# Optimization experiments

Hardware: AMD Instinct MI355X
Metric: run time of the kernel (lower is better)

The kernel has to match this reference:

```python
import jax, jax.numpy as jnp
import numpy as np

C = 256
CQK = C // 8  # 32


def setup_inputs() -> dict:
    key = jax.random.key(0)
    ks = jax.random.split(key, 7)
    x = jax.random.normal(ks[0], (8, C, 64, 64), dtype=jnp.float32)
    s = 1.0 / np.sqrt(C)
    Wq = jax.random.normal(ks[1], (CQK, C), dtype=jnp.float32) * s
    bq = jnp.zeros((CQK,), dtype=jnp.float32)
    Wk = jax.random.normal(ks[2], (CQK, C), dtype=jnp.float32) * s
    bk = jnp.zeros((CQK,), dtype=jnp.float32)
    Wv = jax.random.normal(ks[3], (C, C), dtype=jnp.float32) * s
    bv = jnp.zeros((C,), dtype=jnp.float32)
    gamma = jnp.zeros((1,), dtype=jnp.float32)
    return {"x": x, "Wq": Wq, "bq": bq, "Wk": Wk, "bk": bk, "Wv": Wv, "bv": bv, "gamma": gamma}


def reference(x, Wq, bq, Wk, bk, Wv, bv, gamma):
    B, Cc, H, W = x.shape
    N = H * W
    xf = x.reshape(B, Cc, N)  # [B, C, N]
    # 1x1 convs == channel matmuls
    q = jnp.einsum('oc,bcn->bon', Wq, xf) + bq[None, :, None]  # [B, C//8, N]
    k = jnp.einsum('oc,bcn->bon', Wk, xf) + bk[None, :, None]  # [B, C//8, N]
    v = jnp.einsum('oc,bcn->bon', Wv, xf) + bv[None, :, None]  # [B, C, N]
    scale = float(Cc // 8) ** (-0.5)
    # attention[b, i, j] over keys j (softmax on last dim)
    scores = jnp.einsum('bon,bom->bnm', q, k) * scale  # [B, N, N]
    attn = jax.nn.softmax(scores, axis=-1)
    # out[b,c,i] = sum_j v[b,c,j] * attn[b,i,j]
    out = jnp.einsum('bcj,bij->bci', v, attn).reshape(B, Cc, H, W)
    return gamma * out + x
```

## Files before the change

### kernel.cpp

```cpp
#include <hip/hip_runtime.h>
#include <hip/hip_bf16.h>
#include <math.h>

#define B_   8
#define C_   256
#define N_   4096
#define QSCALE_L2E 0.2550541451582815f
#define DEFER_THR  11.5f

typedef __attribute__((ext_vector_type(8))) short bf16x8;
typedef __attribute__((ext_vector_type(4))) float f32x4;

__device__ __forceinline__ unsigned short bfu(float f) {
    __hip_bfloat16 h = __float2bfloat16(f);
    return __builtin_bit_cast(unsigned short, h);
}
__device__ __forceinline__ unsigned cvtpk(float lo, float hi) {
    unsigned r;
    asm("v_cvt_pk_bf16_f32 %0, %1, %2" : "=v"(r) : "v"(lo), "v"(hi));
    return r;
}

__global__ __launch_bounds__(256) void w_prep(
    const float* __restrict__ Wq, const float* __restrict__ Wk,
    const float* __restrict__ Wv, unsigned short* __restrict__ wbf)
{
    const int i = blockIdx.x * 256 + threadIdx.x;
    const int off = i * 4;
    float4 f;
    if (off < 32 * C_)            f = *reinterpret_cast<const float4*>(Wq + off);
    else if (off < 64 * C_)       f = *reinterpret_cast<const float4*>(Wk + off - 32 * C_);
    else                          f = *reinterpret_cast<const float4*>(Wv + off - 64 * C_);
    ushort4 u;
    u.x = bfu(f.x); u.y = bfu(f.y); u.z = bfu(f.z); u.w = bfu(f.w);
    *reinterpret_cast<ushort4*>(wbf + off) = u;
}

__global__ __launch_bounds__(256, 2) void qkv_proj_mfma(
    const float* __restrict__ x, const unsigned short* __restrict__ wbf,
    const float* __restrict__ bq, const float* __restrict__ bk,
    const float* __restrict__ bv,
    unsigned short* __restrict__ q, unsigned short* __restrict__ k,
    unsigned short* __restrict__ v)
{
    const int b = blockIdx.y, n0 = blockIdx.x * 64;
    const int t = threadIdx.x;
    const int w = t >> 6, l = t & 63;
    const int li = l & 15, g = l >> 4;

    __shared__ unsigned short xT[64 * 256];
    __shared__ unsigned short qkS[2 * 64 * 32];

    {
        const int n = t & 63;
        const int cq0 = t >> 6;
        const float* xb = x + ((size_t)b * C_) * N_ + n0 + n;
        #pragma unroll 4
        for (int s = 0; s < 16; ++s) {
            const int cq = cq0 + 4 * s;
            const float f0 = xb[(size_t)(cq * 4 + 0) * N_];
            const float f1 = xb[(size_t)(cq * 4 + 1) * N_];
            const float f2 = xb[(size_t)(cq * 4 + 2) * N_];
            const float f3 = xb[(size_t)(cq * 4 + 3) * N_];
            ushort4 pk;
            pk.x = bfu(f0); pk.y = bfu(f1); pk.z = bfu(f2); pk.w = bfu(f3);
            const int byte = n * 512 + (((cq >> 1) ^ (n & 7)) << 4) + (cq & 1) * 8;
            *reinterpret_cast<ushort4*>(reinterpret_cast<char*>(xT) + byte) = pk;
        }
    }
    __syncthreads();

    const unsigned short* wq_bf = wbf;
    const unsigned short* wk_bf = wbf + 32 * C_;
    const unsigned short* wv_bf = wbf + 64 * C_;

    const unsigned short* wqk_bf = (w < 2) ? wq_bf : wk_bf;
    const float* bqk = (w < 2) ? bq : bk;
    const float qscl = (w < 2) ? QSCALE_L2E : 1.0f;
    const int mt0 = (w & 1) * 2;
    const int ov0 = w * 64;

    f32x4 accv[4][4];
    f32x4 accq[2][2];
    const f32x4 z4 = {0.f, 0.f, 0.f, 0.f};
    #pragma unroll
    for (int a = 0; a < 4; ++a)
        #pragma unroll
        for (int c2 = 0; c2 < 4; ++c2) accv[a][c2] = z4;
    #pragma unroll
    for (int a = 0; a < 2; ++a)
        #pragma unroll
        for (int c2 = 0; c2 < 2; ++c2) accq[a][c2] = z4;

    #pragma unroll 2
    for (int kk = 0; kk < 8; ++kk) {
        bf16x8 xf[4];
        #pragma unroll
        for (int nt = 0; nt < 4; ++nt) {
            const int row = nt * 16 + li;
            const int byte = row * 512 + (((kk * 4 + g) ^ (row & 7)) << 4);
            xf[nt] = *reinterpret_cast<const bf16x8*>(
                reinterpret_cast<const char*>(xT) + byte);
        }
        #pragma unroll
        for (int ot = 0; ot < 4; ++ot) {
            const bf16x8 wV = *reinterpret_cast<const bf16x8*>(
                wv_bf + (size_t)(ov0 + ot * 16 + li) * C_ + kk * 32 + g * 8);
            #pragma unroll
            for (int nt = 0; nt < 4; ++nt)
                accv[nt][ot] = __builtin_amdgcn_mfma_f32_16x16x32_bf16(
                    xf[nt], wV, accv[nt][ot], 0, 0, 0);
        }
        #pragma unroll
        for (int ot = 0; ot < 2; ++ot) {
            const bf16x8 wA = *reinterpret_cast<const bf16x8*>(
                wqk_bf + (size_t)(ot * 16 + li) * C_ + kk * 32 + g * 8);
            #pragma unroll
            for (int m2 = 0; m2 < 2; ++m2)
                accq[ot][m2] = __builtin_amdgcn_mfma_f32_16x16x32_bf16(
                    wA, xf[mt0 + m2], accq[ot][m2], 0, 0, 0);
        }
    }

    __syncthreads();

    {
        const int qk = (w < 2) ? 0 : 1;
        #pragma unroll
        for (int ot = 0; ot < 2; ++ot) {
            const int d0 = ot * 16 + 4 * g;
            const float4 b4 = *reinterpret_cast<const float4*>(bqk + d0);
            const int slot = ot * 4 + g;
            #pragma unroll
            for (int m2 = 0; m2 < 2; ++m2) {
                const int n = (mt0 + m2) * 16 + li;
                ushort4 s4;
                s4.x = bfu((accq[ot][m2][0] + b4.x) * qscl);
                s4.y = bfu((accq[ot][m2][1] + b4.y) * qscl);
                s4.z = bfu((accq[ot][m2][2] + b4.z) * qscl);
                s4.w = bfu((accq[ot][m2][3] + b4.w) * qscl);
                const int byte = qk * 4096 + n * 64 + ((slot ^ (n & 7)) << 3);
                *reinterpret_cast<ushort4*>(reinterpret_cast<char*>(qkS) + byte) = s4;
            }
        }
    }
    {
        #pragma unroll
        for (int ot = 0; ot < 4; ++ot) {
            const int o = ov0 + ot * 16 + li;
            const float bias = bv[o];
            #pragma unroll
            for (int nt = 0; nt < 4; ++nt) {
                ushort4 s4;
                s4.x = bfu(accv[nt][ot][0] + bias);
                s4.y = bfu(accv[nt][ot][1] + bias);
                s4.z = bfu(accv[nt][ot][2] + bias);
                s4.w = bfu(accv[nt][ot][3] + bias);
                const int slot = nt * 4 + g;
                const int byte = o * 128 + ((slot ^ (o & 7)) << 3);
                *reinterpret_cast<ushort4*>(reinterpret_cast<char*>(xT) + byte) = s4;
            }
        }
    }
    __syncthreads();

    {
        const char* qks = reinterpret_cast<const char*>(qkS);
        #pragma unroll
        for (int qk = 0; qk < 2; ++qk) {
            const int n = t >> 2, s2 = (t & 3) * 2;
            const int byteA = qk * 4096 + n * 64 + (((s2    ) ^ (n & 7)) << 3);
            const int byteB = qk * 4096 + n * 64 + (((s2 + 1) ^ (n & 7)) << 3);
            const uint2 lo = *reinterpret_cast<const uint2*>(qks + byteA);
            const uint2 hi = *reinterpret_cast<const uint2*>(qks + byteB);
            uint4 val = make_uint4(lo.x, lo.y, hi.x, hi.y);
            unsigned short* dst = (qk == 0) ? q : k;
            *reinterpret_cast<uint4*>(dst + ((size_t)b * N_ + n0) * 32 + t * 8) = val;
        }
    }
    {
        const char* vs = reinterpret_cast<const char*>(xT);
        #pragma unroll
        for (int p2 = 0; p2 < 8; ++p2) {
            const int o = p2 * 32 + (t >> 3);
            const int s2 = (t & 7) * 2;
            const int byteA = o * 128 + (((s2    ) ^ (o & 7)) << 3);
            const int byteB = o * 128 + (((s2 + 1) ^ (o & 7)) << 3);
            const uint2 lo = *reinterpret_cast<const uint2*>(vs + byteA);
            const uint2 hi = *reinterpret_cast<const uint2*>(vs + byteB);
            uint4 val = make_uint4(lo.x, lo.y, hi.x, hi.y);
            *reinterpret_cast<uint4*>(v + ((size_t)b * C_ + o) * N_ + n0 + (t & 7) * 8) = val;
        }
    }
}

__global__ __launch_bounds__(256, 2) void attn_mfma(
    const unsigned short* __restrict__ q, const unsigned short* __restrict__ k,
    const unsigned short* __restrict__ v,
    const float* __restrict__ x, const float* __restrict__ gamma,
    float* __restrict__ out)
{
    const int id = blockIdx.x;
    const int b = id & 7;
    const int i0 = (id >> 3) * 64;
    const int t = threadIdx.x;
    const int w = t >> 6, l = t & 63;
    const int li = l & 15, g = l >> 4;

    __shared__ unsigned short kT[2][64 * 32];
    __shared__ unsigned short vT[2][256 * 64];

    const unsigned short* qb = q + (size_t)b * N_ * 32;
    const unsigned short* kb = k + (size_t)b * N_ * 32;
    const unsigned short* vb = v + ((size_t)b * C_) * N_;

    const bf16x8 qf = *reinterpret_cast<const bf16x8*>(
        qb + (size_t)(i0 + w * 16 + li) * 32 + g * 8);

    f32x4 acc[16];
    const f32x4 z4 = {0.f, 0.f, 0.f, 0.f};
    #pragma unroll
    for (int a = 0; a < 16; ++a) acc[a] = z4;

    float m_run = -3.0e38f;
    float l_part = 0.f;

    const int jr = t >> 2, sl = t & 3;
    const int jt_s = jr >> 4, gg = (jr >> 2) & 3, rr = jr & 3;
    const int jperm = (jt_s >> 1) * 32 + (jt_s & 1) * 4 + gg * 8 + rr;
    const int s_src = sl ^ (jr & 3);
    const int koff_sh = jperm * 32 + s_src * 8;
    const unsigned voffK = (unsigned)(koff_sh * 2);
    const int kdst_byte = t * 16;

    const int vrow0 = w * 16 + (l >> 2);
    const int vchunk = l & 3;
    unsigned voffVb[4];
    int vdst[4][2];
    #pragma unroll
    for (int p = 0; p < 4; ++p) {
        const int row = vrow0 + p * 64;
        voffVb[p] = (unsigned)(((size_t)row * N_ + vchunk * 16) * 2);
        const int s0 = vchunk * 2;
        vdst[p][0] = row * 128 + (((s0    ) ^ (row & 7)) << 4);
        vdst[p][1] = row * 128 + (((s0 + 1) ^ (row & 7)) << 4);
    }

    union PB { unsigned wo[4]; bf16x8 v8; };

    {
        const bf16x8 k0 = *reinterpret_cast<const bf16x8*>(
            reinterpret_cast<const char*>(kb) + voffK);
        *reinterpret_cast<bf16x8*>(reinterpret_cast<char*>(&kT[0][0]) + kdst_byte) = k0;
        #pragma unroll
        for (int p = 0; p < 4; ++p) {
            const char* src = reinterpret_cast<const char*>(vb) + voffVb[p];
            const bf16x8 a0 = *reinterpret_cast<const bf16x8*>(src);
            const bf16x8 a1 = *reinterpret_cast<const bf16x8*>(src + 16);
            *reinterpret_cast<bf16x8*>(reinterpret_cast<char*>(&vT[0][0]) + vdst[p][0]) = a0;
            *reinterpret_cast<bf16x8*>(reinterpret_cast<char*>(&vT[0][0]) + vdst[p][1]) = a1;
        }
    }
    __syncthreads();

    for (int jj = 0; jj < 64; ++jj) {
        const int cur = jj & 1, nxt = cur ^ 1;
        const bool pf = (jj + 1 < 64);

        bf16x8 knx;
        bf16x8 vnx[4][2];
        if (pf) {
            const unsigned short* sbk = kb + (size_t)(jj + 1) * 64 * 32;
            asm volatile("global_load_dwordx4 %0, %1, %2"
                         : "=v"(knx) : "v"(voffK), "s"(sbk));
            const unsigned short* sbv = vb + (size_t)(jj + 1) * 64;
            #pragma unroll
            for (int p = 0; p < 4; ++p)
                asm volatile("global_load_dwordx4 %0, %2, %3\n\t"
                             "global_load_dwordx4 %1, %2, %3 offset:16"
                             : "=v"(vnx[p][0]), "=v"(vnx[p][1])
                             : "v"(voffVb[p]), "s"(sbv));
            __builtin_amdgcn_sched_barrier(0);
        }

        f32x4 sT[4];
        {
            const char* kbuf = reinterpret_cast<const char*>(&kT[cur][0]);
            #pragma unroll
            for (int jt = 0; jt < 4; ++jt) {
                const int row = jt * 16 + li;
                const bf16x8 kA = *reinterpret_cast<const bf16x8*>(
                    kbuf + row * 64 + ((g ^ (row & 3)) << 4));
                sT[jt] = __builtin_amdgcn_mfma_f32_16x16x32_bf16(kA, qf, z4, 0, 0, 0);
            }
        }

        float mx = fmaxf(fmaxf(fmaxf(sT[0][0], sT[0][1]), fmaxf(sT[0][2], sT[0][3])),
                         fmaxf(fmaxf(sT[1][0], sT[1][1]), fmaxf(sT[1][2], sT[1][3])));
        mx = fmaxf(mx, fmaxf(fmaxf(fmaxf(sT[2][0], sT[2][1]), fmaxf(sT[2][2], sT[2][3])),
                             fmaxf(fmaxf(sT[3][0], sT[3][1]), fmaxf(sT[3][2], sT[3][3]))));
        if (__any(mx > m_run + DEFER_THR)) {
            float mw = fmaxf(mx, __shfl_xor(mx, 16));
            mw = fmaxf(mw, __shfl_xor(mw, 32));
            const float mnew = fmaxf(m_run, mw);
            const float f = __builtin_amdgcn_exp2f(m_run - mnew);
            m_run = mnew;
            l_part *= f;
            #pragma unroll
            for (int ct = 0; ct < 16; ++ct) acc[ct] *= f;
        }
        #pragma unroll
        for (int jt = 0; jt < 4; ++jt)
            #pragma unroll
            for (int r = 0; r < 4; ++r)
                sT[jt][r] = __builtin_amdgcn_exp2f(sT[jt][r] - m_run);
        const f32x4 sv = (sT[0] + sT[1]) + (sT[2] + sT[3]);
        l_part += (sv[0] + sv[1]) + (sv[2] + sv[3]);

        PB pb0, pb1;
        pb0.wo[0] = cvtpk(sT[0][0], sT[0][1]); pb0.wo[1] = cvtpk(sT[0][2], sT[0][3]);
        pb0.wo[2] = cvtpk(sT[1][0], sT[1][1]); pb0.wo[3] = cvtpk(sT[1][2], sT[1][3]);
        pb1.wo[0] = cvtpk(sT[2][0], sT[2][1]); pb1.wo[1] = cvtpk(sT[2][2], sT[2][3]);
        pb1.wo[2] = cvtpk(sT[3][0], sT[3][1]); pb1.wo[3] = cvtpk(sT[3][2], sT[3][3]);

        __builtin_amdgcn_s_setprio(1);
        {
            const char* vbuf = reinterpret_cast<const char*>(&vT[cur][0]);
            #pragma unroll
            for (int ct = 0; ct < 16; ++ct) {
                const int vrow = ct * 16 + li;
                const bf16x8 vA0 = *reinterpret_cast<const bf16x8*>(
                    vbuf + vrow * 128 + (((g    ) ^ (vrow & 7)) << 4));
                const bf16x8 vA1 = *reinterpret_cast<const bf16x8*>(
                    vbuf + vrow * 128 + (((4 + g) ^ (vrow & 7)) << 4));
                acc[ct] = __builtin_amdgcn_mfma_f32_16x16x32_bf16(vA0, pb0.v8, acc[ct], 0, 0, 0);
                acc[ct] = __builtin_amdgcn_mfma_f32_16x16x32_bf16(vA1, pb1.v8, acc[ct], 0, 0, 0);
            }
        }
        __builtin_amdgcn_s_setprio(0);

        if (pf) {
            asm volatile("s_waitcnt vmcnt(0)" ::: "memory");
            __builtin_amdgcn_sched_barrier(0);
            *reinterpret_cast<bf16x8*>(
                reinterpret_cast<char*>(&kT[nxt][0]) + kdst_byte) = knx;
            char* vd = reinterpret_cast<char*>(&vT[nxt][0]);
            #pragma unroll
            for (int p = 0; p < 4; ++p) {
                *reinterpret_cast<bf16x8*>(vd + vdst[p][0]) = vnx[p][0];
                *reinterpret_cast<bf16x8*>(vd + vdst[p][1]) = vnx[p][1];
            }
        }
        __syncthreads();
    }

    float l_tot = l_part;
    l_tot += __shfl_xor(l_tot, 16);
    l_tot += __shfl_xor(l_tot, 32);
    const float linv = 1.0f / l_tot;

    const float gm = gamma[0];
    const int i = i0 + w * 16 + li;
    const float* xb2 = x + ((size_t)b * C_) * N_ + i;
    float* ob = out + ((size_t)b * C_) * N_ + i;
    #pragma unroll
    for (int ct = 0; ct < 16; ++ct) {
        #pragma unroll
        for (int r = 0; r < 4; ++r) {
            const int c = ct * 16 + 4 * g + r;
            const size_t off = (size_t)c * N_;
            ob[off] = gm * acc[ct][r] * linv + xb2[off];
        }
    }
}

extern "C" void kernel_launch(void* const* d_in, const int* in_sizes, int n_in,
                              void* d_out, int out_size, void* d_ws, size_t ws_size,
                              hipStream_t stream) {
    const float* x     = (const float*)d_in[0];
    const float* Wq    = (const float*)d_in[1];
    const float* bq    = (const float*)d_in[2];
    const float* Wk    = (const float*)d_in[3];
    const float* bk    = (const float*)d_in[4];
    const float* Wv    = (const float*)d_in[5];
    const float* bv    = (const float*)d_in[6];
    const float* gamma = (const float*)d_in[7];
    float* out = (float*)d_out;

    unsigned short* q   = (unsigned short*)d_ws;
    unsigned short* k   = q + (size_t)B_ * N_ * 32;
    unsigned short* v   = k + (size_t)B_ * N_ * 32;
    unsigned short* wbf = v + (size_t)B_ * C_ * N_;

    dim3 grid(N_ / 64, B_);
    w_prep<<<80, 256, 0, stream>>>(Wq, Wk, Wv, wbf);
    qkv_proj_mfma<<<grid, 256, 0, stream>>>(x, wbf, bq, bk, bv, q, k, v);
    attn_mfma<<<512, 256, 0, stream>>>(q, k, v, x, gamma, out);
}
```

Measured before the change: 156.2 us.

## Process two query tiles per wave to reuse K/V LDS fragments

Each wave now handles 32 query rows as two 16-row sub-tiles (A and B), so each K and V fragment read from LDS feeds two MFMAs. The block covers 128 queries and the grid is halved to 256 blocks. The aim is to halve K/V global and LDS traffic per query. In exchange it doubles accumulator registers, drops launch bounds to 1 block per SM, and leaves only 256 blocks for 256 CUs, which reduces occupancy and latency hiding.

```diff
diff --git a/kernel.cpp b/kernel.cpp
--- a/kernel.cpp
+++ b/kernel.cpp
@@ -194,7 +194,7 @@
     }
 }
 
-__global__ __launch_bounds__(256, 2) void attn_mfma(
+__global__ __launch_bounds__(256, 1) void attn_mfma(
     const unsigned short* __restrict__ q, const unsigned short* __restrict__ k,
     const unsigned short* __restrict__ v,
     const float* __restrict__ x, const float* __restrict__ gamma,
@@ -202,7 +202,7 @@
 {
     const int id = blockIdx.x;
     const int b = id & 7;
-    const int i0 = (id >> 3) * 64;
+    const int i0 = (id >> 3) * 128;
     const int t = threadIdx.x;
     const int w = t >> 6, l = t & 63;
     const int li = l & 15, g = l >> 4;
@@ -214,16 +214,18 @@
     const unsigned short* kb = k + (size_t)b * N_ * 32;
     const unsigned short* vb = v + ((size_t)b * C_) * N_;
 
-    const bf16x8 qf = *reinterpret_cast<const bf16x8*>(
-        qb + (size_t)(i0 + w * 16 + li) * 32 + g * 8);
-
-    f32x4 acc[16];
+    const bf16x8 qfA = *reinterpret_cast<const bf16x8*>(
+        qb + (size_t)(i0 + w * 32 + li) * 32 + g * 8);
+    const bf16x8 qfB = *reinterpret_cast<const bf16x8*>(
+        qb + (size_t)(i0 + w * 32 + 16 + li) * 32 + g * 8);
+
+    f32x4 accA[16], accB[16];
     const f32x4 z4 = {0.f, 0.f, 0.f, 0.f};
     #pragma unroll
-    for (int a = 0; a < 16; ++a) acc[a] = z4;
-
-    float m_run = -3.0e38f;
-    float l_part = 0.f;
+    for (int a = 0; a < 16; ++a) { accA[a] = z4; accB[a] = z4; }
+
+    float m_runA = -3.0e38f, m_runB = -3.0e38f;
+    float l_pA = 0.f, l_pB = 0.f;
 
     const int jr = t >> 2, sl = t & 3;
     const int jt_s = jr >> 4, gg = (jr >> 2) & 3, rr = jr & 3;
@@ -283,7 +285,7 @@
             __builtin_amdgcn_sched_barrier(0);
         }
 
-        f32x4 sT[4];
+        f32x4 sTA[4], sTB[4];
         {
             const char* kbuf = reinterpret_cast<const char*>(&kT[cur][0]);
             #pragma unroll
@@ -291,37 +293,56 @@
                 const int row = jt * 16 + li;
                 const bf16x8 kA = *reinterpret_cast<const bf16x8*>(
                     kbuf + row * 64 + ((g ^ (row & 3)) << 4));
-                sT[jt] = __builtin_amdgcn_mfma_f32_16x16x32_bf16(kA, qf, z4, 0, 0, 0);
-            }
-        }
-
-        float mx = fmaxf(fmaxf(fmaxf(sT[0][0], sT[0][1]), fmaxf(sT[0][2], sT[0][3])),
-                         fmaxf(fmaxf(sT[1][0], sT[1][1]), fmaxf(sT[1][2], sT[1][3])));
-        mx = fmaxf(mx, fmaxf(fmaxf(fmaxf(sT[2][0], sT[2][1]), fmaxf(sT[2][2], sT[2][3])),
-                             fmaxf(fmaxf(sT[3][0], sT[3][1]), fmaxf(sT[3][2], sT[3][3]))));
-        if (__any(mx > m_run + DEFER_THR)) {
-            float mw = fmaxf(mx, __shfl_xor(mx, 16));
-            mw = fmaxf(mw, __shfl_xor(mw, 32));
-            const float mnew = fmaxf(m_run, mw);
-            const float f = __builtin_amdgcn_exp2f(m_run - mnew);
-            m_run = mnew;
-            l_part *= f;
-            #pragma unroll
-            for (int ct = 0; ct < 16; ++ct) acc[ct] *= f;
+                sTA[jt] = __builtin_amdgcn_mfma_f32_16x16x32_bf16(kA, qfA, z4, 0, 0, 0);
+                sTB[jt] = __builtin_amdgcn_mfma_f32_16x16x32_bf16(kA, qfB, z4, 0, 0, 0);
+            }
+        }
+
+        float mxA = fmaxf(fmaxf(fmaxf(sTA[0][0], sTA[0][1]), fmaxf(sTA[0][2], sTA[0][3])),
+                          fmaxf(fmaxf(sTA[1][0], sTA[1][1]), fmaxf(sTA[1][2], sTA[1][3])));
+        mxA = fmaxf(mxA, fmaxf(fmaxf(fmaxf(sTA[2][0], sTA[2][1]), fmaxf(sTA[2][2], sTA[2][3])),
+                               fmaxf(fmaxf(sTA[3][0], sTA[3][1]), fmaxf(sTA[3][2], sTA[3][3]))));
+        float mxB = fmaxf(fmaxf(fmaxf(sTB[0][0], sTB[0][1]), fmaxf(sTB[0][2], sTB[0][3])),
+                          fmaxf(fmaxf(sTB[1][0], sTB[1][1]), fmaxf(sTB[1][2], sTB[1][3])));
+        mxB = fmaxf(mxB, fmaxf(fmaxf(fmaxf(sTB[2][0], sTB[2][1]), fmaxf(sTB[2][2], sTB[2][3])),
+                               fmaxf(fmaxf(sTB[3][0], sTB[3][1]), fmaxf(sTB[3][2], sTB[3][3]))));
+        if (__any(fmaxf(mxA - m_runA, mxB - m_runB) > DEFER_THR)) {
+            float mwA = fmaxf(mxA, __shfl_xor(mxA, 16));
+            mwA = fmaxf(mwA, __shfl_xor(mwA, 32));
+            float mwB = fmaxf(mxB, __shfl_xor(mxB, 16));
+            mwB = fmaxf(mwB, __shfl_xor(mwB, 32));
+            const float mnA = fmaxf(m_runA, mwA);
+            const float mnB = fmaxf(m_runB, mwB);
+            const float fA = __builtin_amdgcn_exp2f(m_runA - mnA);
+            const float fB = __builtin_amdgcn_exp2f(m_runB - mnB);
+            m_runA = mnA; m_runB = mnB;
+            l_pA *= fA;   l_pB *= fB;
+            #pragma unroll
+            for (int ct = 0; ct < 16; ++ct) { accA[ct] *= fA; accB[ct] *= fB; }
         }
         #pragma unroll
         for (int jt = 0; jt < 4; ++jt)
             #pragma unroll
-            for (int r = 0; r < 4; ++r)
-                sT[jt][r] = __builtin_amdgcn_exp2f(sT[jt][r] - m_run);
-        const f32x4 sv = (sT[0] + sT[1]) + (sT[2] + sT[3]);
-        l_part += (sv[0] + sv[1]) + (sv[2] + sv[3]);
-
-        PB pb0, pb1;
-        pb0.wo[0] = cvtpk(sT[0][0], sT[0][1]); pb0.wo[1] = cvtpk(sT[0][2], sT[0][3]);
-        pb0.wo[2] = cvtpk(sT[1][0], sT[1][1]); pb0.wo[3] = cvtpk(sT[1][2], sT[1][3]);
-        pb1.wo[0] = cvtpk(sT[2][0], sT[2][1]); pb1.wo[1] = cvtpk(sT[2][2], sT[2][3]);
-        pb1.wo[2] = cvtpk(sT[3][0], sT[3][1]); pb1.wo[3] = cvtpk(sT[3][2], sT[3][3]);
+            for (int r = 0; r < 4; ++r) {
+                sTA[jt][r] = __builtin_amdgcn_exp2f(sTA[jt][r] - m_runA);
+                sTB[jt][r] = __builtin_amdgcn_exp2f(sTB[jt][r] - m_runB);
+            }
+        {
+            const f32x4 svA = (sTA[0] + sTA[1]) + (sTA[2] + sTA[3]);
+            const f32x4 svB = (sTB[0] + sTB[1]) + (sTB[2] + sTB[3]);
+            l_pA += (svA[0] + svA[1]) + (svA[2] + svA[3]);
+            l_pB += (svB[0] + svB[1]) + (svB[2] + svB[3]);
+        }
+
+        PB pbA0, pbA1, pbB0, pbB1;
+        pbA0.wo[0] = cvtpk(sTA[0][0], sTA[0][1]); pbA0.wo[1] = cvtpk(sTA[0][2], sTA[0][3]);
+        pbA0.wo[2] = cvtpk(sTA[1][0], sTA[1][1]); pbA0.wo[3] = cvtpk(sTA[1][2], sTA[1][3]);
+        pbA1.wo[0] = cvtpk(sTA[2][0], sTA[2][1]); pbA1.wo[1] = cvtpk(sTA[2][2], sTA[2][3]);
+        pbA1.wo[2] = cvtpk(sTA[3][0], sTA[3][1]); pbA1.wo[3] = cvtpk(sTA[3][2], sTA[3][3]);
+        pbB0.wo[0] = cvtpk(sTB[0][0], sTB[0][1]); pbB0.wo[1] = cvtpk(sTB[0][2], sTB[0][3]);
+        pbB0.wo[2] = cvtpk(sTB[1][0], sTB[1][1]); pbB0.wo[3] = cvtpk(sTB[1][2], sTB[1][3]);
+        pbB1.wo[0] = cvtpk(sTB[2][0], sTB[2][1]); pbB1.wo[1] = cvtpk(sTB[2][2], sTB[2][3]);
+        pbB1.wo[2] = cvtpk(sTB[3][0], sTB[3][1]); pbB1.wo[3] = cvtpk(sTB[3][2], sTB[3][3]);
 
         __builtin_amdgcn_s_setprio(1);
         {
@@ -333,8 +354,10 @@
                     vbuf + vrow * 128 + (((g    ) ^ (vrow & 7)) << 4));
                 const bf16x8 vA1 = *reinterpret_cast<const bf16x8*>(
                     vbuf + vrow * 128 + (((4 + g) ^ (vrow & 7)) << 4));
-                acc[ct] = __builtin_amdgcn_mfma_f32_16x16x32_bf16(vA0, pb0.v8, acc[ct], 0, 0, 0);
-                acc[ct] = __builtin_amdgcn_mfma_f32_16x16x32_bf16(vA1, pb1.v8, acc[ct], 0, 0, 0);
+                accA[ct] = __builtin_amdgcn_mfma_f32_16x16x32_bf16(vA0, pbA0.v8, accA[ct], 0, 0, 0);
+                accB[ct] = __builtin_amdgcn_mfma_f32_16x16x32_bf16(vA0, pbB0.v8, accB[ct], 0, 0, 0);
+                accA[ct] = __builtin_amdgcn_mfma_f32_16x16x32_bf16(vA1, pbA1.v8, accA[ct], 0, 0, 0);
+                accB[ct] = __builtin_amdgcn_mfma_f32_16x16x32_bf16(vA1, pbB1.v8, accB[ct], 0, 0, 0);
             }
         }
         __builtin_amdgcn_s_setprio(0);
@@ -354,22 +377,24 @@
         __syncthreads();
     }
 
-    float l_tot = l_part;
-    l_tot += __shfl_xor(l_tot, 16);
-    l_tot += __shfl_xor(l_tot, 32);
-    const float linv = 1.0f / l_tot;
+    float lA = l_pA, lB = l_pB;
+    lA += __shfl_xor(lA, 16); lA += __shfl_xor(lA, 32);
+    lB += __shfl_xor(lB, 16); lB += __shfl_xor(lB, 32);
+    const float linvA = 1.0f / lA;
+    const float linvB = 1.0f / lB;
 
     const float gm = gamma[0];
-    const int i = i0 + w * 16 + li;
-    const float* xb2 = x + ((size_t)b * C_) * N_ + i;
-    float* ob = out + ((size_t)b * C_) * N_ + i;
+    const int iA = i0 + w * 32 + li;
+    const float* xb2 = x + ((size_t)b * C_) * N_;
+    float* ob = out + ((size_t)b * C_) * N_;
     #pragma unroll
     for (int ct = 0; ct < 16; ++ct) {
         #pragma unroll
         for (int r = 0; r < 4; ++r) {
             const int c = ct * 16 + 4 * g + r;
-            const size_t off = (size_t)c * N_;
-            ob[off] = gm * acc[ct][r] * linv + xb2[off];
+            const size_t offA = (size_t)c * N_ + iA;
+            ob[offA]      = gm * accA[ct][r] * linvA + xb2[offA];
+            ob[offA + 16] = gm * accB[ct][r] * linvB + xb2[offA + 16];
         }
     }
 }
@@ -395,5 +420,5 @@
     dim3 grid(N_ / 64, B_);
     w_prep<<<80, 256, 0, stream>>>(Wq, Wk, Wv, wbf);
     qkv_proj_mfma<<<grid, 256, 0, stream>>>(x, wbf, bq, bk, bv, q, k, v);
-    attn_mfma<<<512, 256, 0, stream>>>(q, k, v, x, gamma, out);
-}
+    attn_mfma<<<256, 256, 0, stream>>>(q, k, v, x, gamma, out);
+}
```

Measured after the change: 175.7 us. 1.12x slower.
